# Performance work log

Measured on AMD Instinct MI355X. Metric: run time of the kernel, lower is better.

The kernel has to match this reference:

```python
import jax, jax.numpy as jnp
import numpy as np

B, LQ, LK, D, H = 4, 1024, 1024, 512, 8


def setup_inputs() -> dict:
    key = jax.random.key(0)
    ks = jax.random.split(key, 6)
    # xavier_normal for (D, D): std = sqrt(2 / (D + D))
    std_qkv = (2.0 / (D + D)) ** 0.5
    std_p = (2.0 / (H * D + D)) ** 0.5
    x = jax.random.normal(ks[0], (B, LQ, D), dtype=jnp.float32)
    states = jax.random.normal(ks[1], (B, LK, D), dtype=jnp.float32)
    mask = jnp.ones((B, LQ, LK), dtype=jnp.int32)
    # per-head full-size QKV weights, stacked over heads: [H, D, D]
    Wq = jax.random.normal(ks[2], (H, D, D), dtype=jnp.float32) * std_qkv
    Wk = jax.random.normal(ks[3], (H, D, D), dtype=jnp.float32) * std_qkv
    Wv = jax.random.normal(ks[4], (H, D, D), dtype=jnp.float32) * std_qkv
    Wp = jax.random.normal(ks[5], (D, H * D), dtype=jnp.float32) * std_p
    return {"x": x, "states": states, "mask": mask,
            "Wq": Wq, "Wk": Wk, "Wv": Wv, "Wp": Wp}


def reference(x, states, mask, Wq, Wk, Wv, Wp):
    # Per-head linear projections (nn.Linear: y = x @ W.T), batched over heads.
    q = jnp.einsum('bld,hed->bhle', x, Wq)        # [B,H,Lq,D]
    k = jnp.einsum('bsd,hed->bhse', states, Wk)   # [B,H,Lk,D]
    v = jnp.einsum('bsd,hed->bhse', states, Wv)   # [B,H,Lk,D]
    scale = 1.0 / (D ** 0.5)
    scores = jnp.einsum('bhle,bhse->bhls', q, k) * scale  # [B,H,Lq,Lk]
    scores = jnp.where(mask[:, None, :, :] == 0, -jnp.inf, scores)
    attn = jax.nn.softmax(scores, axis=-1)
    # Original does broadcast multiply + sum; mathematically this is attn @ v.
    ctx = jnp.einsum('bhls,bhse->bhle', attn, v)  # [B,H,Lq,D]
    # torch.cat over heads in order -> head-major last dim
    ctx = jnp.transpose(ctx, (0, 2, 1, 3)).reshape(B, LQ, H * D)
    return ctx @ Wp.T  # [B,Lq,D]
```

## Files before the change

kernel.cpp:

```cpp
#include <hip/hip_runtime.h>
#include <hip/hip_bf16.h>
#include <cstdint>
#include <cstddef>


typedef __bf16 bf16;
typedef __bf16 bf16x4 __attribute__((ext_vector_type(4)));
typedef __bf16 bf16x8 __attribute__((ext_vector_type(8)));
typedef float f32x4 __attribute__((ext_vector_type(4)));

__device__ inline void gload_lds16(const void* g, void* l) {
  __builtin_amdgcn_global_load_lds(
      (const __attribute__((address_space(1))) void*)g,
      (__attribute__((address_space(3))) void*)l, 16, 0, 0);
}

template <typename CT, int MODE>
__device__ __forceinline__ void gemm256(
    bf16* lds,
    const bf16* __restrict__ A, const bf16* __restrict__ B, CT* __restrict__ C,
    int K, int lda, int ldb, int ldc, int m0, int n0, float scale,
    const unsigned* __restrict__ mrow, float* __restrict__ sumrow)
{
  const int t = threadIdx.x;
  const int lane = t & 63;
  const int w = t >> 6;
  const int wm = w >> 2, wn = w & 3;
  const int rr = lane & 15, q4 = lane >> 4;

  const int tr = t >> 2;
  const int tc = (t & 3) ^ (tr & 3);
  const bf16* Ag = A + (size_t)(m0 + tr) * lda + tc * 8;
  const bf16* Bg = B + (size_t)(n0 + tr) * ldb + tc * 8;
  bf16* ldsSt = lds + t * 8;

  const int nT = K >> 5;

  auto stageA = [&](int tt) {
    bf16* d = ldsSt + (tt & 3) * 16384;
    const bf16* s = Ag + tt * 32;
    gload_lds16(s, d);
    gload_lds16(s + (size_t)128 * lda, d + 4096);
  };
  auto stageB = [&](int tt) {
    bf16* d = ldsSt + (tt & 3) * 16384 + 8192;
    const bf16* s = Bg + tt * 32;
    gload_lds16(s, d);
    gload_lds16(s + (size_t)128 * ldb, d + 4096);
  };

  stageA(0); stageB(0);
  stageA(1); stageB(1);
  stageA(2); stageB(2);
  asm volatile("s_waitcnt vmcnt(8)" ::: "memory");
  __builtin_amdgcn_s_barrier();
  __builtin_amdgcn_sched_barrier(0);

  f32x4 acc[8][4] = {};

  for (int tt = 0; tt < nT; ++tt) {
    const bf16* Al = lds + (tt & 3) * 16384;
    const bf16* Bl = Al + 8192;
    bf16x8 af[4], bg[4];

#pragma unroll
    for (int m = 0; m < 4; ++m) {
      const int R = wm * 128 + m * 16 + rr;
      af[m] = *(const bf16x8*)(Al + R * 32 + ((q4 ^ (R & 3)) << 3));
    }
#pragma unroll
    for (int n = 0; n < 4; ++n) {
      const int R = wn * 64 + n * 16 + rr;
      bg[n] = *(const bf16x8*)(Bl + R * 32 + ((q4 ^ (R & 3)) << 3));
    }
    if (tt + 3 < nT) stageA(tt + 3);
    __builtin_amdgcn_s_barrier();
    __builtin_amdgcn_sched_barrier(0);
    __builtin_amdgcn_s_setprio(1);
#pragma unroll
    for (int m = 0; m < 4; ++m)
#pragma unroll
      for (int n = 0; n < 4; ++n)
        acc[m][n] = __builtin_amdgcn_mfma_f32_16x16x32_bf16(af[m], bg[n], acc[m][n], 0, 0, 0);
    __builtin_amdgcn_s_setprio(0);
    __builtin_amdgcn_s_barrier();
    __builtin_amdgcn_sched_barrier(0);

#pragma unroll
    for (int m = 0; m < 4; ++m) {
      const int R = wm * 128 + 64 + m * 16 + rr;
      af[m] = *(const bf16x8*)(Al + R * 32 + ((q4 ^ (R & 3)) << 3));
    }
    if (tt + 3 < nT) stageB(tt + 3);
    __builtin_amdgcn_s_barrier();
    __builtin_amdgcn_sched_barrier(0);
    __builtin_amdgcn_s_setprio(1);
#pragma unroll
    for (int m = 0; m < 4; ++m)
#pragma unroll
      for (int n = 0; n < 4; ++n)
        acc[4 + m][n] = __builtin_amdgcn_mfma_f32_16x16x32_bf16(af[m], bg[n], acc[4 + m][n], 0, 0, 0);
    __builtin_amdgcn_s_setprio(0);

    const int rem = nT - tt;
    if (rem > 3)       asm volatile("s_waitcnt vmcnt(8)" ::: "memory");
    else if (rem == 3) asm volatile("s_waitcnt vmcnt(4)" ::: "memory");
    else               asm volatile("s_waitcnt vmcnt(0)" ::: "memory");
    __builtin_amdgcn_s_barrier();
    __builtin_amdgcn_sched_barrier(0);
  }

  if (MODE == 0) {
#pragma unroll
    for (int m = 0; m < 8; ++m) {
#pragma unroll
      for (int n = 0; n < 4; ++n) {
        const int gr0 = m0 + wm * 128 + m * 16 + (q4 << 2);
        const int gc = n0 + wn * 64 + n * 16 + rr;
#pragma unroll
        for (int i = 0; i < 4; ++i)
          C[(size_t)(gr0 + i) * ldc + gc] = (CT)(acc[m][n][i] * scale);
      }
    }
  } else if (MODE == 1) {
    const int cb0 = (n0 + wn * 64) >> 5;
#pragma unroll
    for (int m = 0; m < 8; ++m) {
#pragma unroll
      for (int i = 0; i < 4; ++i) {
        const int row = m0 + wm * 128 + m * 16 + (q4 << 2) + i;
        const unsigned mw0 = mrow[(row << 5) + cb0];
        const unsigned mw1 = mrow[(row << 5) + cb0 + 1];
        float ps = 0.0f;
#pragma unroll
        for (int n = 0; n < 4; ++n) {
          const int gc = n0 + wn * 64 + n * 16 + rr;
          const unsigned mw = (n >= 2) ? mw1 : mw0;
          const unsigned bit = (mw >> (((n & 1) << 4) + rr)) & 1u;
          float p = bit ? __expf(acc[m][n][i] * scale) : 0.0f;
          C[(size_t)row * ldc + gc] = (CT)p;
          ps += p;
        }
        ps += __shfl_xor(ps, 1); ps += __shfl_xor(ps, 2);
        ps += __shfl_xor(ps, 4); ps += __shfl_xor(ps, 8);
        if (rr == 0) atomicAdd(sumrow + row, ps);
      }
    }
  } else {
#pragma unroll
    for (int m = 0; m < 8; ++m) {
      const int gr0 = m0 + wm * 128 + m * 16 + (q4 << 2);
      float inv[4];
#pragma unroll
      for (int i = 0; i < 4; ++i) inv[i] = 1.0f / sumrow[gr0 + i];
#pragma unroll
      for (int n = 0; n < 4; ++n) {
        const int gc = n0 + wn * 64 + n * 16 + rr;
#pragma unroll
        for (int i = 0; i < 4; ++i)
          C[(size_t)(gr0 + i) * ldc + gc] = (CT)(acc[m][n][i] * inv[i]);
      }
    }
  }
}

__global__ __launch_bounds__(256) void prep_kernel(
    const float* __restrict__ x, const float* __restrict__ st,
    const float* __restrict__ Wq, const float* __restrict__ Wk,
    const float* __restrict__ Wp, const float* __restrict__ Wv,
    const int* __restrict__ mask,
    bf16* __restrict__ xb, bf16* __restrict__ stb, bf16* __restrict__ wqb,
    bf16* __restrict__ wkb, bf16* __restrict__ wpb, bf16* __restrict__ WvT,
    unsigned* __restrict__ mbits, float* __restrict__ sums)
{
  const int lin = blockIdx.x;
  const int t = threadIdx.x;
  if (lin < 10240) {
    const float* s; bf16* d;
    switch (lin >> 11) {
      case 0: s = x; d = xb; break;
      case 1: s = st; d = stb; break;
      case 2: s = Wq; d = wqb; break;
      case 3: s = Wk; d = wkb; break;
      default: s = Wp; d = wpb; break;
    }
    const int i = ((lin & 2047) * 256 + t) * 4;
    float4 v = *(const float4*)(s + i);
    bf16x4 o;
    o[0] = (bf16)v.x; o[1] = (bf16)v.y; o[2] = (bf16)v.z; o[3] = (bf16)v.w;
    *(bf16x4*)(d + i) = o;
  } else if (lin < 12288) {
    const int gid = (lin - 10240) * 256 + t;
    const int e0 = (gid & 127) * 4;
    const int d = (gid >> 7) & 511;
    const int h = gid >> 16;
    const float* src = Wv + (size_t)h * 262144 + (size_t)e0 * 512 + d;
    bf16x4 o;
    o[0] = (bf16)src[0];
    o[1] = (bf16)src[512];
    o[2] = (bf16)src[1024];
    o[3] = (bf16)src[1536];
    *(bf16x4*)(WvT + (size_t)h * 262144 + (size_t)d * 512 + e0) = o;
  } else if (lin < 12800) {
    const int gid = (lin - 12288) * 256 + t;
    const int* src = mask + (size_t)gid * 32;
    unsigned bits = 0;
#pragma unroll
    for (int j = 0; j < 32; j += 4) {
      int4 v = *(const int4*)(src + j);
      if (v.x) bits |= 1u << j;
      if (v.y) bits |= 1u << (j + 1);
      if (v.z) bits |= 1u << (j + 2);
      if (v.w) bits |= 1u << (j + 3);
    }
    mbits[gid] = bits;
  } else {
    const int i = ((lin - 12800) * 256 + t) * 4;
    *(float4*)(sums + i) = make_float4(0.f, 0.f, 0.f, 0.f);
  }
}

__global__ __launch_bounds__(512, 2) void proj_kernel(
    const bf16* __restrict__ xb, const bf16* __restrict__ stb,
    const bf16* __restrict__ wqb, const bf16* __restrict__ wkb,
    const bf16* __restrict__ wpb, const bf16* __restrict__ WvT,
    bf16* __restrict__ q, bf16* __restrict__ k, bf16* __restrict__ U)
{
  __shared__ bf16 lds[65536];
  const int bid = blockIdx.x;
  const int g = (bid & 7) * 68 + (bid >> 3);
  if (g < 512) {
    const int z = g >> 3;
    const int tile = g & 7;
    const int job = z >> 5;
    const int zz = z & 31;
    const size_t zb = zz >> 3, zh = zz & 7;
    const bf16* Ain = job ? stb : xb;
    const bf16* W = job ? wkb : wqb;
    bf16* Cout = job ? k : q;
    gemm256<bf16, 0>(lds, Ain + zb * 524288, W + zh * 262144,
        Cout + zb * 4194304 + zh * 524288, 512, 512, 512, 512,
        (tile >> 1) * 256, (tile & 1) * 256, 1.0f, nullptr, nullptr);
  } else {
    const int g2 = g - 512;
    const int h = g2 >> 2;
    const int tile = g2 & 3;
    gemm256<bf16, 0>(lds, wpb + (size_t)h * 512, WvT + (size_t)h * 262144,
        U + (size_t)h * 262144, 512, 4096, 512, 512,
        (tile >> 1) * 256, (tile & 1) * 256, 1.0f, nullptr, nullptr);
  }
}

__global__ __launch_bounds__(512, 2) void big_kernel(
    const bf16* __restrict__ q, const bf16* __restrict__ k,
    const bf16* __restrict__ U, const bf16* __restrict__ stb,
    bf16* __restrict__ P, bf16* __restrict__ VWT,
    const unsigned* __restrict__ mbits, float* __restrict__ sums, float scale)
{
  __shared__ bf16 lds[65536];
  const int bid = blockIdx.x;
  const int g = (bid & 7) * 96 + (bid >> 3);
  if (g < 512) {
    const int z = g >> 4;
    const int tile = g & 15;
    const size_t zb = z >> 3, zh = z & 7;
    gemm256<bf16, 1>(lds,
        q + zb * 4194304 + zh * 524288,
        k + zb * 4194304 + zh * 524288,
        P + zb * 8388608 + zh * 1048576,
        512, 512, 512, 1024,
        (tile >> 2) * 256, (tile & 3) * 256, scale,
        mbits + (zb << 15), sums + ((size_t)z << 10));
  } else {
    const int g2 = g - 512;
    const int z = g2 >> 3;
    const int tile = g2 & 7;
    const size_t zb = z >> 3, zh = z & 7;
    gemm256<bf16, 0>(lds, U + zh * 262144, stb + zb * 524288,
        VWT + zb * 4194304 + zh * 524288, 512, 512, 512, 1024,
        (tile >> 2) * 256, (tile & 3) * 256, 1.0f, nullptr, nullptr);
  }
}

__global__ __launch_bounds__(512, 2) void pvw_kernel(
    const bf16* __restrict__ P, const bf16* __restrict__ VWT,
    float* __restrict__ sums, float* __restrict__ part)
{
  __shared__ bf16 lds[65536];
  const int bid = blockIdx.x;
  const int g = (bid & 7) * 32 + (bid >> 3);
  const int z = g >> 3;
  const int tile = g & 7;
  const size_t zb = z >> 3, zh = z & 7;
  gemm256<float, 2>(lds,
      P + zb * 8388608 + zh * 1048576,
      VWT + zb * 4194304 + zh * 524288,
      part + zh * 2097152 + zb * 524288,
      1024, 1024, 1024, 512,
      (tile >> 1) * 256, (tile & 1) * 256, 1.0f,
      nullptr, sums + ((size_t)z << 10));
}

__global__ __launch_bounds__(256) void reduce8(
    const float* __restrict__ part, float* __restrict__ out)
{
  const size_t i = ((size_t)blockIdx.x * 256 + threadIdx.x) * 4;
  float4 o = *(const float4*)(part + i);
#pragma unroll
  for (int h = 1; h < 8; ++h) {
    float4 a = *(const float4*)(part + (size_t)h * 2097152 + i);
    o.x += a.x; o.y += a.y; o.z += a.z; o.w += a.w;
  }
  *(float4*)(out + i) = o;
}

extern "C" void kernel_launch(void* const* d_in, const int* in_sizes, int n_in,
                              void* d_out, int out_size, void* d_ws, size_t ws_size,
                              hipStream_t stream) {
  const float* x    = (const float*)d_in[0];
  const float* st   = (const float*)d_in[1];
  const int*   mask = (const int*)d_in[2];
  const float* Wq   = (const float*)d_in[3];
  const float* Wk   = (const float*)d_in[4];
  const float* Wv   = (const float*)d_in[5];
  const float* Wp   = (const float*)d_in[6];
  float* out = (float*)d_out;

  char* ws = (char*)d_ws;
  const size_t MB = 1048576;
  bf16* xb  = (bf16*)(ws);
  bf16* stb = (bf16*)(ws + 4 * MB);
  bf16* wqb = (bf16*)(ws + 8 * MB);
  bf16* wkb = (bf16*)(ws + 12 * MB);
  bf16* wpb = (bf16*)(ws + 16 * MB);
  bf16* WvT = (bf16*)(ws + 20 * MB);
  bf16* U   = (bf16*)(ws + 24 * MB);
  bf16* q   = (bf16*)(ws + 28 * MB);
  bf16* k   = (bf16*)(ws + 60 * MB);
  bf16* VWT = (bf16*)(ws + 92 * MB);
  bf16* sc  = (bf16*)(ws + 124 * MB);
  unsigned* mbits = (unsigned*)(ws + 188 * MB);
  float*    sums  = (float*)(ws + 189 * MB);
  float*    part  = (float*)(ws + 28 * MB);

  const float scale = 0.04419417382415922f;

  prep_kernel<<<dim3(12832), dim3(256), 0, stream>>>(x, st, Wq, Wk, Wp, Wv, mask,
      xb, stb, wqb, wkb, wpb, WvT, mbits, sums);

  proj_kernel<<<dim3(544), dim3(512), 0, stream>>>(xb, stb, wqb, wkb, wpb, WvT,
      q, k, U);

  big_kernel<<<dim3(768), dim3(512), 0, stream>>>(q, k, U, stb, sc, VWT,
      mbits, sums, scale);

  pvw_kernel<<<dim3(256), dim3(512), 0, stream>>>(sc, VWT, sums, part);

  reduce8<<<dim3(2048), dim3(256), 0, stream>>>(part, out);
}
```

Before: 333.5 us.

## Switch GEMM main loop to BK=64 double-buffer with four-phase ping-pong schedule

Restructures the 256x256 GEMM inner loop from a 4-stage ring of K=32 tiles to a 2-stage double buffer of K=64 tiles. It uses an 8-way XOR swizzle and splits each iteration into four MFMA quadrants, with global-to-LDS prefetch of the next tile interleaved between them. The aim is fewer barriers per unit of K and better overlap of loads with MFMA work. In exchange, prefetch depth drops to one tile, which raises exposure to load latency and adds fragment registers.

```diff
diff --git a/kernel.cpp b/kernel.cpp
--- a/kernel.cpp
+++ b/kernel.cpp
@@ -14,6 +14,8 @@
       (const __attribute__((address_space(1))) void*)g,
       (__attribute__((address_space(3))) void*)l, 16, 0, 0);
 }
+
+#define SBAR0 __builtin_amdgcn_sched_barrier(0)
 
 template <typename CT, int MODE>
 __device__ __forceinline__ void gemm256(
@@ -28,86 +30,128 @@
   const int wm = w >> 2, wn = w & 3;
   const int rr = lane & 15, q4 = lane >> 4;
 
-  const int tr = t >> 2;
-  const int tc = (t & 3) ^ (tr & 3);
-  const bf16* Ag = A + (size_t)(m0 + tr) * lda + tc * 8;
-  const bf16* Bg = B + (size_t)(n0 + tr) * ldb + tc * 8;
-  bf16* ldsSt = lds + t * 8;
-
-  const int nT = K >> 5;
-
-  auto stageA = [&](int tt) {
-    bf16* d = ldsSt + (tt & 3) * 16384;
-    const bf16* s = Ag + tt * 32;
-    gload_lds16(s, d);
-    gload_lds16(s + (size_t)128 * lda, d + 4096);
+  const int s64row = t >> 3;
+  const int ssl    = t & 7;
+  const int s64ch  = ssl ^ (s64row & 7);
+  const int tb     = t & 255;
+  const int sbrow  = tb >> 3;
+  const int sbch   = ssl ^ (sbrow & 7);
+  const int hb     = t >> 8;
+
+  const int nT = K >> 6;
+
+  auto stageA = [&](int tt, int row0) {
+    const int r = row0 + s64row;
+    gload_lds16(A + (size_t)(m0 + r) * lda + tt * 64 + s64ch * 8,
+                lds + (tt & 1) * 32768 + row0 * 64 + t * 8);
   };
-  auto stageB = [&](int tt) {
-    bf16* d = ldsSt + (tt & 3) * 16384 + 8192;
-    const bf16* s = Bg + tt * 32;
-    gload_lds16(s, d);
-    gload_lds16(s + (size_t)128 * ldb, d + 4096);
+  auto stageB = [&](int tt, int b0) {
+    const int r = b0 + hb * 64 + sbrow;
+    gload_lds16(B + (size_t)(n0 + r) * ldb + tt * 64 + sbch * 8,
+                lds + (tt & 1) * 32768 + 16384 + r * 64 + ssl * 8);
   };
 
-  stageA(0); stageB(0);
-  stageA(1); stageB(1);
-  stageA(2); stageB(2);
-  asm volatile("s_waitcnt vmcnt(8)" ::: "memory");
+  stageA(0, 0);   stageA(0, 128);
+  stageB(0, 0);   stageB(0, 128);
+  stageB(0, 32);  stageB(0, 160);
+  stageA(0, 64);  stageA(0, 192);
+  SBAR0;
+  asm volatile("s_waitcnt vmcnt(4)" ::: "memory");
   __builtin_amdgcn_s_barrier();
-  __builtin_amdgcn_sched_barrier(0);
+  SBAR0;
 
   f32x4 acc[8][4] = {};
+  bf16x8 af[2][4];
+  bf16x8 bgf[2][4];
+
+  const int sw0 = (q4 ^ (rr & 7)) << 3;
+  const int sw1 = sw0 ^ 32;
 
   for (int tt = 0; tt < nT; ++tt) {
-    const bf16* Al = lds + (tt & 3) * 16384;
-    const bf16* Bl = Al + 8192;
-    bf16x8 af[4], bg[4];
+    const bf16* Ab = lds + (tt & 1) * 32768 + (wm * 128 + rr) * 64;
+    const bf16* Bb = lds + (tt & 1) * 32768 + 16384 + (wn * 64 + rr) * 64;
+    const bool pf = (tt + 1) < nT;
 
 #pragma unroll
     for (int m = 0; m < 4; ++m) {
-      const int R = wm * 128 + m * 16 + rr;
-      af[m] = *(const bf16x8*)(Al + R * 32 + ((q4 ^ (R & 3)) << 3));
-    }
-#pragma unroll
-    for (int n = 0; n < 4; ++n) {
-      const int R = wn * 64 + n * 16 + rr;
-      bg[n] = *(const bf16x8*)(Bl + R * 32 + ((q4 ^ (R & 3)) << 3));
-    }
-    if (tt + 3 < nT) stageA(tt + 3);
+      af[0][m] = *(const bf16x8*)(Ab + m * 1024 + sw0);
+      af[1][m] = *(const bf16x8*)(Ab + m * 1024 + sw1);
+    }
+#pragma unroll
+    for (int n = 0; n < 2; ++n) {
+      bgf[0][n] = *(const bf16x8*)(Bb + n * 1024 + sw0);
+      bgf[1][n] = *(const bf16x8*)(Bb + n * 1024 + sw1);
+    }
+    if (pf) { stageA(tt + 1, 0); stageA(tt + 1, 128); }
+    SBAR0;
+    if (pf) asm volatile("s_waitcnt vmcnt(4)" ::: "memory");
+    else    asm volatile("s_waitcnt vmcnt(2)" ::: "memory");
     __builtin_amdgcn_s_barrier();
-    __builtin_amdgcn_sched_barrier(0);
+    SBAR0;
     __builtin_amdgcn_s_setprio(1);
 #pragma unroll
-    for (int m = 0; m < 4; ++m)
-#pragma unroll
-      for (int n = 0; n < 4; ++n)
-        acc[m][n] = __builtin_amdgcn_mfma_f32_16x16x32_bf16(af[m], bg[n], acc[m][n], 0, 0, 0);
+    for (int kk = 0; kk < 2; ++kk)
+#pragma unroll
+      for (int m = 0; m < 4; ++m)
+#pragma unroll
+        for (int n = 0; n < 2; ++n)
+          acc[m][n] = __builtin_amdgcn_mfma_f32_16x16x32_bf16(af[kk][m], bgf[kk][n], acc[m][n], 0, 0, 0);
     __builtin_amdgcn_s_setprio(0);
+
+#pragma unroll
+    for (int n = 2; n < 4; ++n) {
+      bgf[0][n] = *(const bf16x8*)(Bb + n * 1024 + sw0);
+      bgf[1][n] = *(const bf16x8*)(Bb + n * 1024 + sw1);
+    }
+    if (pf) { stageB(tt + 1, 0); stageB(tt + 1, 128); }
+    SBAR0;
+    if (pf) asm volatile("s_waitcnt vmcnt(4)" ::: "memory");
+    else    asm volatile("s_waitcnt vmcnt(0)" ::: "memory");
     __builtin_amdgcn_s_barrier();
-    __builtin_amdgcn_sched_barrier(0);
+    SBAR0;
+    __builtin_amdgcn_s_setprio(1);
+#pragma unroll
+    for (int kk = 0; kk < 2; ++kk)
+#pragma unroll
+      for (int m = 0; m < 4; ++m)
+#pragma unroll
+        for (int n = 2; n < 4; ++n)
+          acc[m][n] = __builtin_amdgcn_mfma_f32_16x16x32_bf16(af[kk][m], bgf[kk][n], acc[m][n], 0, 0, 0);
+    __builtin_amdgcn_s_setprio(0);
 
 #pragma unroll
     for (int m = 0; m < 4; ++m) {
-      const int R = wm * 128 + 64 + m * 16 + rr;
-      af[m] = *(const bf16x8*)(Al + R * 32 + ((q4 ^ (R & 3)) << 3));
-    }
-    if (tt + 3 < nT) stageB(tt + 3);
+      af[0][m] = *(const bf16x8*)(Ab + (64 + m * 16) * 64 + sw0);
+      af[1][m] = *(const bf16x8*)(Ab + (64 + m * 16) * 64 + sw1);
+    }
+    if (pf) { stageB(tt + 1, 32); stageB(tt + 1, 160); }
+    SBAR0;
     __builtin_amdgcn_s_barrier();
-    __builtin_amdgcn_sched_barrier(0);
+    SBAR0;
     __builtin_amdgcn_s_setprio(1);
 #pragma unroll
-    for (int m = 0; m < 4; ++m)
-#pragma unroll
-      for (int n = 0; n < 4; ++n)
-        acc[4 + m][n] = __builtin_amdgcn_mfma_f32_16x16x32_bf16(af[m], bg[n], acc[4 + m][n], 0, 0, 0);
+    for (int kk = 0; kk < 2; ++kk)
+#pragma unroll
+      for (int m = 0; m < 4; ++m)
+#pragma unroll
+        for (int n = 0; n < 2; ++n)
+          acc[4 + m][n] = __builtin_amdgcn_mfma_f32_16x16x32_bf16(af[kk][m], bgf[kk][n], acc[4 + m][n], 0, 0, 0);
     __builtin_amdgcn_s_setprio(0);
 
-    const int rem = nT - tt;
-    if (rem > 3)       asm volatile("s_waitcnt vmcnt(8)" ::: "memory");
-    else if (rem == 3) asm volatile("s_waitcnt vmcnt(4)" ::: "memory");
-    else               asm volatile("s_waitcnt vmcnt(0)" ::: "memory");
+    if (pf) { stageA(tt + 1, 64); stageA(tt + 1, 192); }
+    SBAR0;
+    if (pf) asm volatile("s_waitcnt vmcnt(4)" ::: "memory");
     __builtin_amdgcn_s_barrier();
-    __builtin_amdgcn_sched_barrier(0);
+    SBAR0;
+    __builtin_amdgcn_s_setprio(1);
+#pragma unroll
+    for (int kk = 0; kk < 2; ++kk)
+#pragma unroll
+      for (int m = 0; m < 4; ++m)
+#pragma unroll
+        for (int n = 2; n < 4; ++n)
+          acc[4 + m][n] = __builtin_amdgcn_mfma_f32_16x16x32_bf16(af[kk][m], bgf[kk][n], acc[4 + m][n], 0, 0, 0);
+    __builtin_amdgcn_s_setprio(0);
   }
 
   if (MODE == 0) {
```

After: 315.9 us. 5.3% less time.

## Replace 256x256 GEMM tiles with 128x128 tiles and BK=64 double buffering

Applied to the files above, without the earlier changes.

Replaces the 256x256, 8-wave GEMM core with a 128x128, 4-wave tile that uses a K-step of 64, a two-stage LDS double buffer, an XOR swizzle over 8 chunks, and a compile-time K so the loop fully unrolls. Grid sizes grow fourfold and LDS use per block halves, aiming at better CU occupancy and load balance on 256 CUs (e.g. pvw previously had only 256 blocks). The cost is lower arithmetic intensity per tile, more global traffic, and a shallower prefetch pipeline.

```diff
diff --git a/kernel.cpp b/kernel.cpp
--- a/kernel.cpp
+++ b/kernel.cpp
@@ -15,107 +15,93 @@
       (__attribute__((address_space(3))) void*)l, 16, 0, 0);
 }
 
-template <typename CT, int MODE>
-__device__ __forceinline__ void gemm256(
+#define SBAR0 __builtin_amdgcn_sched_barrier(0)
+
+template <typename CT, int MODE, int K>
+__device__ __forceinline__ void gemm128(
     bf16* lds,
     const bf16* __restrict__ A, const bf16* __restrict__ B, CT* __restrict__ C,
-    int K, int lda, int ldb, int ldc, int m0, int n0, float scale,
+    int lda, int ldb, int ldc, int m0, int n0, float scale,
     const unsigned* __restrict__ mrow, float* __restrict__ sumrow)
 {
   const int t = threadIdx.x;
   const int lane = t & 63;
   const int w = t >> 6;
-  const int wm = w >> 2, wn = w & 3;
+  const int wm = w >> 1, wn = w & 1;
   const int rr = lane & 15, q4 = lane >> 4;
 
-  const int tr = t >> 2;
-  const int tc = (t & 3) ^ (tr & 3);
-  const bf16* Ag = A + (size_t)(m0 + tr) * lda + tc * 8;
-  const bf16* Bg = B + (size_t)(n0 + tr) * ldb + tc * 8;
-  bf16* ldsSt = lds + t * 8;
-
-  const int nT = K >> 5;
-
-  auto stageA = [&](int tt) {
-    bf16* d = ldsSt + (tt & 3) * 16384;
-    const bf16* s = Ag + tt * 32;
-    gload_lds16(s, d);
-    gload_lds16(s + (size_t)128 * lda, d + 4096);
+  const int srow = t >> 3;
+  const int ssl  = t & 7;
+  const int sch  = ssl ^ (srow & 7);
+  constexpr int nT = K >> 6;
+
+  const bf16* Ag = A + (size_t)(m0 + srow) * lda + sch * 8;
+  const bf16* Bg = B + (size_t)(n0 + srow) * ldb + sch * 8;
+  bf16* std_ = lds + t * 8;
+
+  auto stage = [&](int tt) {
+    const bf16* As = Ag + tt * 64;
+    const bf16* Bs = Bg + tt * 64;
+    bf16* d = std_ + (tt & 1) * 16384;
+#pragma unroll
+    for (int i = 0; i < 4; ++i) {
+      gload_lds16(As + (size_t)(32 * i) * lda, d + i * 2048);
+      gload_lds16(Bs + (size_t)(32 * i) * ldb, d + 8192 + i * 2048);
+    }
   };
-  auto stageB = [&](int tt) {
-    bf16* d = ldsSt + (tt & 3) * 16384 + 8192;
-    const bf16* s = Bg + tt * 32;
-    gload_lds16(s, d);
-    gload_lds16(s + (size_t)128 * ldb, d + 4096);
-  };
-
-  stageA(0); stageB(0);
-  stageA(1); stageB(1);
-  stageA(2); stageB(2);
-  asm volatile("s_waitcnt vmcnt(8)" ::: "memory");
-  __builtin_amdgcn_s_barrier();
-  __builtin_amdgcn_sched_barrier(0);
-
-  f32x4 acc[8][4] = {};
-
+
+  stage(0);
+
+  f32x4 acc[4][4] = {};
+
+  const int sw0 = (q4 ^ (rr & 7)) << 3;
+  const int sw1 = sw0 ^ 32;
+
+#pragma unroll
   for (int tt = 0; tt < nT; ++tt) {
-    const bf16* Al = lds + (tt & 3) * 16384;
-    const bf16* Bl = Al + 8192;
-    bf16x8 af[4], bg[4];
-
+    const bool pf = (tt + 1) < nT;
+
+    if (pf) stage(tt + 1);
+    if (pf) asm volatile("s_waitcnt vmcnt(8)" ::: "memory");
+    else    asm volatile("s_waitcnt vmcnt(0)" ::: "memory");
+    __builtin_amdgcn_s_barrier();
+    SBAR0;
+
+    const bf16* Ab = lds + (tt & 1) * 16384 + (wm * 64 + rr) * 64;
+    const bf16* Bb = lds + (tt & 1) * 16384 + 8192 + (wn * 64 + rr) * 64;
+    bf16x8 af[2][4], bg[2][4];
 #pragma unroll
     for (int m = 0; m < 4; ++m) {
-      const int R = wm * 128 + m * 16 + rr;
-      af[m] = *(const bf16x8*)(Al + R * 32 + ((q4 ^ (R & 3)) << 3));
+      af[0][m] = *(const bf16x8*)(Ab + m * 1024 + sw0);
+      af[1][m] = *(const bf16x8*)(Ab + m * 1024 + sw1);
     }
 #pragma unroll
     for (int n = 0; n < 4; ++n) {
-      const int R = wn * 64 + n * 16 + rr;
-      bg[n] = *(const bf16x8*)(Bl + R * 32 + ((q4 ^ (R & 3)) << 3));
-    }
-    if (tt + 3 < nT) stageA(tt + 3);
+      bg[0][n] = *(const bf16x8*)(Bb + n * 1024 + sw0);
+      bg[1][n] = *(const bf16x8*)(Bb + n * 1024 + sw1);
+    }
+    asm volatile("s_waitcnt lgkmcnt(0)" ::: "memory");
+    SBAR0;
+
+    __builtin_amdgcn_s_setprio(1);
+#pragma unroll
+    for (int kk = 0; kk < 2; ++kk)
+#pragma unroll
+      for (int m = 0; m < 4; ++m)
+#pragma unroll
+        for (int n = 0; n < 4; ++n)
+          acc[m][n] = __builtin_amdgcn_mfma_f32_16x16x32_bf16(af[kk][m], bg[kk][n], acc[m][n], 0, 0, 0);
+    __builtin_amdgcn_s_setprio(0);
+
     __builtin_amdgcn_s_barrier();
-    __builtin_amdgcn_sched_barrier(0);
-    __builtin_amdgcn_s_setprio(1);
-#pragma unroll
-    for (int m = 0; m < 4; ++m)
-#pragma unroll
-      for (int n = 0; n < 4; ++n)
-        acc[m][n] = __builtin_amdgcn_mfma_f32_16x16x32_bf16(af[m], bg[n], acc[m][n], 0, 0, 0);
-    __builtin_amdgcn_s_setprio(0);
-    __builtin_amdgcn_s_barrier();
-    __builtin_amdgcn_sched_barrier(0);
-
+  }
+
+  if (MODE == 0) {
 #pragma unroll
     for (int m = 0; m < 4; ++m) {
-      const int R = wm * 128 + 64 + m * 16 + rr;
-      af[m] = *(const bf16x8*)(Al + R * 32 + ((q4 ^ (R & 3)) << 3));
-    }
-    if (tt + 3 < nT) stageB(tt + 3);
-    __builtin_amdgcn_s_barrier();
-    __builtin_amdgcn_sched_barrier(0);
-    __builtin_amdgcn_s_setprio(1);
-#pragma unroll
-    for (int m = 0; m < 4; ++m)
-#pragma unroll
-      for (int n = 0; n < 4; ++n)
-        acc[4 + m][n] = __builtin_amdgcn_mfma_f32_16x16x32_bf16(af[m], bg[n], acc[4 + m][n], 0, 0, 0);
-    __builtin_amdgcn_s_setprio(0);
-
-    const int rem = nT - tt;
-    if (rem > 3)       asm volatile("s_waitcnt vmcnt(8)" ::: "memory");
-    else if (rem == 3) asm volatile("s_waitcnt vmcnt(4)" ::: "memory");
-    else               asm volatile("s_waitcnt vmcnt(0)" ::: "memory");
-    __builtin_amdgcn_s_barrier();
-    __builtin_amdgcn_sched_barrier(0);
-  }
-
-  if (MODE == 0) {
-#pragma unroll
-    for (int m = 0; m < 8; ++m) {
 #pragma unroll
       for (int n = 0; n < 4; ++n) {
-        const int gr0 = m0 + wm * 128 + m * 16 + (q4 << 2);
+        const int gr0 = m0 + wm * 64 + m * 16 + (q4 << 2);
         const int gc = n0 + wn * 64 + n * 16 + rr;
 #pragma unroll
         for (int i = 0; i < 4; ++i)
@@ -125,10 +111,10 @@
   } else if (MODE == 1) {
     const int cb0 = (n0 + wn * 64) >> 5;
 #pragma unroll
-    for (int m = 0; m < 8; ++m) {
+    for (int m = 0; m < 4; ++m) {
 #pragma unroll
       for (int i = 0; i < 4; ++i) {
-        const int row = m0 + wm * 128 + m * 16 + (q4 << 2) + i;
+        const int row = m0 + wm * 64 + m * 16 + (q4 << 2) + i;
         const unsigned mw0 = mrow[(row << 5) + cb0];
         const unsigned mw1 = mrow[(row << 5) + cb0 + 1];
         float ps = 0.0f;
@@ -148,8 +134,8 @@
     }
   } else {
 #pragma unroll
-    for (int m = 0; m < 8; ++m) {
-      const int gr0 = m0 + wm * 128 + m * 16 + (q4 << 2);
+    for (int m = 0; m < 4; ++m) {
+      const int gr0 = m0 + wm * 64 + m * 16 + (q4 << 2);
       float inv[4];
 #pragma unroll
       for (int i = 0; i < 4; ++i) inv[i] = 1.0f / sumrow[gr0 + i];
@@ -220,84 +206,84 @@
   }
 }
 
-__global__ __launch_bounds__(512, 2) void proj_kernel(
+__global__ __launch_bounds__(256, 2) void proj_kernel(
     const bf16* __restrict__ xb, const bf16* __restrict__ stb,
     const bf16* __restrict__ wqb, const bf16* __restrict__ wkb,
     const bf16* __restrict__ wpb, const bf16* __restrict__ WvT,
     bf16* __restrict__ q, bf16* __restrict__ k, bf16* __restrict__ U)
 {
-  __shared__ bf16 lds[65536];
+  __shared__ bf16 lds[32768];
   const int bid = blockIdx.x;
-  const int g = (bid & 7) * 68 + (bid >> 3);
-  if (g < 512) {
-    const int z = g >> 3;
-    const int tile = g & 7;
+  const int g = (bid & 7) * 272 + (bid >> 3);
+  if (g < 2048) {
+    const int z = g >> 5;
+    const int tile = g & 31;
     const int job = z >> 5;
     const int zz = z & 31;
     const size_t zb = zz >> 3, zh = zz & 7;
     const bf16* Ain = job ? stb : xb;
     const bf16* W = job ? wkb : wqb;
     bf16* Cout = job ? k : q;
-    gemm256<bf16, 0>(lds, Ain + zb * 524288, W + zh * 262144,
-        Cout + zb * 4194304 + zh * 524288, 512, 512, 512, 512,
-        (tile >> 1) * 256, (tile & 1) * 256, 1.0f, nullptr, nullptr);
+    gemm128<bf16, 0, 512>(lds, Ain + zb * 524288, W + zh * 262144,
+        Cout + zb * 4194304 + zh * 524288, 512, 512, 512,
+        (tile >> 2) * 128, (tile & 3) * 128, 1.0f, nullptr, nullptr);
   } else {
-    const int g2 = g - 512;
-    const int h = g2 >> 2;
-    const int tile = g2 & 3;
-    gemm256<bf16, 0>(lds, wpb + (size_t)h * 512, WvT + (size_t)h * 262144,
-        U + (size_t)h * 262144, 512, 4096, 512, 512,
-        (tile >> 1) * 256, (tile & 1) * 256, 1.0f, nullptr, nullptr);
-  }
-}
-
-__global__ __launch_bounds__(512, 2) void big_kernel(
+    const int g2 = g - 2048;
+    const int h = g2 >> 4;
+    const int tile = g2 & 15;
+    gemm128<bf16, 0, 512>(lds, wpb + (size_t)h * 512, WvT + (size_t)h * 262144,
+        U + (size_t)h * 262144, 4096, 512, 512,
+        (tile >> 2) * 128, (tile & 3) * 128, 1.0f, nullptr, nullptr);
+  }
+}
+
+__global__ __launch_bounds__(256, 2) void big_kernel(
     const bf16* __restrict__ q, const bf16* __restrict__ k,
     const bf16* __restrict__ U, const bf16* __restrict__ stb,
     bf16* __restrict__ P, bf16* __restrict__ VWT,
     const unsigned* __restrict__ mbits, float* __restrict__ sums, float scale)
 {
-  __shared__ bf16 lds[65536];
+  __shared__ bf16 lds[32768];
   const int bid = blockIdx.x;
-  const int g = (bid & 7) * 96 + (bid >> 3);
-  if (g < 512) {
-    const int z = g >> 4;
-    const int tile = g & 15;
+  const int g = (bid & 7) * 384 + (bid >> 3);
+  if (g < 2048) {
+    const int z = g >> 6;
+    const int tile = g & 63;
     const size_t zb = z >> 3, zh = z & 7;
-    gemm256<bf16, 1>(lds,
+    gemm128<bf16, 1, 512>(lds,
         q + zb * 4194304 + zh * 524288,
         k + zb * 4194304 + zh * 524288,
         P + zb * 8388608 + zh * 1048576,
-        512, 512, 512, 1024,
-        (tile >> 2) * 256, (tile & 3) * 256, scale,
+        512, 512, 1024,
+        (tile >> 3) * 128, (tile & 7) * 128, scale,
         mbits + (zb << 15), sums + ((size_t)z << 10));
   } else {
-    const int g2 = g - 512;
-    const int z = g2 >> 3;
-    const int tile = g2 & 7;
+    const int g2 = g - 2048;
+    const int z = g2 >> 5;
+    const int tile = g2 & 31;
     const size_t zb = z >> 3, zh = z & 7;
-    gemm256<bf16, 0>(lds, U + zh * 262144, stb + zb * 524288,
-        VWT + zb * 4194304 + zh * 524288, 512, 512, 512, 1024,
-        (tile >> 2) * 256, (tile & 3) * 256, 1.0f, nullptr, nullptr);
-  }
-}
-
-__global__ __launch_bounds__(512, 2) void pvw_kernel(
+    gemm128<bf16, 0, 512>(lds, U + zh * 262144, stb + zb * 524288,
+        VWT + zb * 4194304 + zh * 524288, 512, 512, 1024,
+        (tile >> 3) * 128, (tile & 7) * 128, 1.0f, nullptr, nullptr);
+  }
+}
+
+__global__ __launch_bounds__(256, 2) void pvw_kernel(
     const bf16* __restrict__ P, const bf16* __restrict__ VWT,
     float* __restrict__ sums, float* __restrict__ part)
 {
-  __shared__ bf16 lds[65536];
+  __shared__ bf16 lds[32768];
   const int bid = blockIdx.x;
-  const int g = (bid & 7) * 32 + (bid >> 3);
-  const int z = g >> 3;
-  const int tile = g & 7;
+  const int g = (bid & 7) * 128 + (bid >> 3);
+  const int z = g >> 5;
+  const int tile = g & 31;
   const size_t zb = z >> 3, zh = z & 7;
-  gemm256<float, 2>(lds,
+  gemm128<float, 2, 1024>(lds,
       P + zb * 8388608 + zh * 1048576,
       VWT + zb * 4194304 + zh * 524288,
       part + zh * 2097152 + zb * 524288,
-      1024, 1024, 1024, 512,
-      (tile >> 1) * 256, (tile & 1) * 256, 1.0f,
+      1024, 1024, 512,
+      (tile >> 2) * 128, (tile & 3) * 128, 1.0f,
       nullptr, sums + ((size_t)z << 10));
 }
 
@@ -348,13 +334,13 @@
   prep_kernel<<<dim3(12832), dim3(256), 0, stream>>>(x, st, Wq, Wk, Wp, Wv, mask,
       xb, stb, wqb, wkb, wpb, WvT, mbits, sums);
 
-  proj_kernel<<<dim3(544), dim3(512), 0, stream>>>(xb, stb, wqb, wkb, wpb, WvT,
+  proj_kernel<<<dim3(2176), dim3(256), 0, stream>>>(xb, stb, wqb, wkb, wpb, WvT,
       q, k, U);
 
-  big_kernel<<<dim3(768), dim3(512), 0, stream>>>(q, k, U, stb, sc, VWT,
+  big_kernel<<<dim3(3072), dim3(256), 0, stream>>>(q, k, U, stb, sc, VWT,
       mbits, sums, scale);
 
-  pvw_kernel<<<dim3(256), dim3(512), 0, stream>>>(sc, VWT, sums, part);
+  pvw_kernel<<<dim3(1024), dim3(256), 0, stream>>>(sc, VWT, sums, part);
 
   reduce8<<<dim3(2048), dim3(256), 0, stream>>>(part, out);
 }
```

Result: faster. 303.9 us (-8.9%).
